# Optimization experiments

Hardware: AMD Instinct MI355X
Metric: run time of the kernel (lower is better)

Reference implementation:

```python
import jax, jax.numpy as jnp
import numpy as np

CHEB_K = 3
ORDER = 2


def setup_inputs() -> dict:
    key = jax.random.key(0)
    ks = jax.random.split(key, 7)
    B, C, N, T = 16, 64, 2048, 12
    E, O = 10, 64
    x = jax.random.normal(ks[0], (B, C, N, T), jnp.float32)
    node_embeddings = jax.random.normal(ks[1], (N, E), jnp.float32)
    # nonnegative row-normalized adjacency for the diffusion branch
    a = jax.random.uniform(ks[2], (1, N, N), jnp.float32)
    support = a / jnp.sum(a, axis=-1, keepdims=True)
    weights_pool = 0.05 * jax.random.normal(ks[3], (E, CHEB_K, C, O), jnp.float32)
    bias_pool = 0.05 * jax.random.normal(ks[4], (E, O), jnp.float32)
    mlp_w = 0.05 * jax.random.normal(ks[5], ((ORDER * 1 + 1) * C, O), jnp.float32)
    mlp_b = 0.05 * jax.random.normal(ks[6], (O,), jnp.float32)
    return {
        "x": x,
        "node_embeddings": node_embeddings,
        "support": support,
        "weights_pool": weights_pool,
        "bias_pool": bias_pool,
        "mlp_w": mlp_w,
        "mlp_b": mlp_b,
    }


def reference(x, node_embeddings, support, weights_pool, bias_pool, mlp_w, mlp_b):
    # ---- adaptive Chebyshev branch ----
    N = node_embeddings.shape[0]
    A = jax.nn.softmax(jax.nn.relu(node_embeddings @ node_embeddings.T), axis=1)  # [N,N]
    supports = [jnp.eye(N, dtype=A.dtype), A]
    for _ in range(2, CHEB_K):
        supports.append(2.0 * (A @ supports[-1]) - supports[-2])
    S = jnp.stack(supports, axis=0)                         # [K,N,N]
    weights = jnp.einsum('nd,dkio->nkio', node_embeddings, weights_pool)  # [N,K,C,O]
    bias = node_embeddings @ bias_pool                      # [N,O]
    # x: [B,C,N,T]; diffuse then contract per-node weights
    x_g = jnp.einsum('knm,bimw->bwnki', S, x)               # [B,T,N,K,C]
    x_av = jnp.einsum('bwnki,nkio->bwno', x_g, weights) + bias  # [B,T,N,O]
    x_av = x_av.transpose(0, 3, 2, 1)                       # [B,O,N,T]

    # ---- diffusion conv branch ----
    out = [x]
    for si in range(support.shape[0]):
        a = support[si]                                     # [N,N]
        x1 = jnp.einsum('bcvl,vw->bcwl', x, a)
        out.append(x1)
        for _ in range(2, ORDER + 1):
            x1 = jnp.einsum('bcvl,vw->bcwl', x1, a)
            out.append(x1)
    xg = jnp.concatenate(out, axis=1)                       # [B,(order*S+1)*C,N,T]
    # 1x1 Conv2d == channel matmul; dropout is identity in eval mode
    x_gcn = jnp.einsum('bcnw,co->bonw', xg, mlp_w) + mlp_b[None, :, None, None]
    return x_av, x_gcn
```

## Files before the change

kernel.cpp:

```cpp
#include <hip/hip_runtime.h>
#include <stdint.h>

#define NN    2048
#define BB    16
#define CC    64
#define TT    12
#define OO    64
#define ED    10
#define JJ    12288
#define NJ    25165824
#define KC    192
#define NTK   32

typedef __attribute__((ext_vector_type(8))) short short8;
typedef __attribute__((ext_vector_type(4))) float f32x4;

__device__ __forceinline__ unsigned short f2bf(float x) {
    union { float f; unsigned int u; } v; v.f = x;
    unsigned int r = (v.u + 0x7FFFu + ((v.u >> 16) & 1u)) >> 16;
    return (unsigned short)r;
}
__device__ __forceinline__ float bf2f(unsigned short h) {
    union { unsigned int u; float f; } v; v.u = ((unsigned int)h) << 16;
    return v.f;
}
__device__ __forceinline__ void async_cp16(const void* g, void* l) {
    __builtin_amdgcn_global_load_lds(
        (const __attribute__((address_space(1))) void*)(uintptr_t)g,
        (__attribute__((address_space(3))) void*)(uintptr_t)l, 16, 0, 0);
}

__global__ __launch_bounds__(256) void k_softmax_A(const float* __restrict__ E,
                                                   unsigned short* __restrict__ Abf) {
    int n = blockIdx.x, tid = threadIdx.x;
    __shared__ float row[NN];
    __shared__ float red[256];
    float en[ED];
#pragma unroll
    for (int d = 0; d < ED; ++d) en[d] = E[n * ED + d];
    float mx = 0.0f;
    for (int m = tid; m < NN; m += 256) {
        float s = 0.f;
#pragma unroll
        for (int d = 0; d < ED; ++d) s += en[d] * E[m * ED + d];
        s = fmaxf(s, 0.0f);
        row[m] = s;
        mx = fmaxf(mx, s);
    }
    red[tid] = mx; __syncthreads();
    for (int s = 128; s; s >>= 1) { if (tid < s) red[tid] = fmaxf(red[tid], red[tid + s]); __syncthreads(); }
    mx = red[0]; __syncthreads();
    float sum = 0.f;
    for (int m = tid; m < NN; m += 256) { float e = __expf(row[m] - mx); row[m] = e; sum += e; }
    red[tid] = sum; __syncthreads();
    for (int s = 128; s; s >>= 1) { if (tid < s) red[tid] += red[tid + s]; __syncthreads(); }
    float inv = 1.0f / red[0];
    for (int m = tid; m < NN; m += 256) Abf[(size_t)n * NN + m] = f2bf(row[m] * inv);
}

__global__ void k_trans_bf(const float* __restrict__ src, unsigned short* __restrict__ dst) {
    __shared__ float t[32][33];
    int tx = threadIdx.x, ty = threadIdx.y;
    int x0 = blockIdx.x * 32, y0 = blockIdx.y * 32;
#pragma unroll
    for (int i = 0; i < 4; ++i)
        t[ty + i * 8][tx] = src[(size_t)(y0 + ty + i * 8) * NN + x0 + tx];
    __syncthreads();
#pragma unroll
    for (int i = 0; i < 4; ++i)
        dst[(size_t)(x0 + ty + i * 8) * NN + y0 + tx] = f2bf(t[tx][ty + i * 8]);
}

__global__ __launch_bounds__(256) void k_make_X2b(const float* __restrict__ x,
                                                  unsigned short* __restrict__ X2,
                                                  unsigned short* __restrict__ X2t) {
    extern __shared__ float lx[];
    int b = blockIdx.x, n0 = blockIdx.y * 32, tid = threadIdx.x;
#pragma unroll
    for (int v = 0; v < 24; ++v) {
        int f4 = v * 256 + tid;
        int c = f4 / 96, r4 = f4 - c * 96;
        const float4* src = (const float4*)(x + ((size_t)(b * CC + c) * NN + n0) * TT) + r4;
        float4 val = *src;
#pragma unroll
        for (int u = 0; u < 4; ++u) {
            int idx = r4 * 4 + u;
            int n = idx / 12, t = idx - n * 12;
            lx[c * 417 + n * 13 + t] = ((const float*)&val)[u];
        }
    }
    __syncthreads();
#pragma unroll
    for (int v = 0; v < 12; ++v) {
        int flat = v * 256 + tid;
        int n = flat / 96, u8 = flat - n * 96;
        int jl = u8 * 8;
        int t = jl >> 6, c0 = jl & 63;
        unsigned short w[8];
#pragma unroll
        for (int e = 0; e < 8; ++e) w[e] = f2bf(lx[(c0 + e) * 417 + n * 13 + t]);
        *(short8*)&X2[(size_t)(n0 + n) * JJ + b * 768 + jl] = *(short8*)w;
    }
#pragma unroll
    for (int v = 0; v < 12; ++v) {
        int flat = v * 256 + tid;
        int jl = flat >> 2, nq = (flat & 3) * 8;
        int t = jl >> 6, c = jl & 63;
        unsigned short w[8];
#pragma unroll
        for (int e = 0; e < 8; ++e) w[e] = f2bf(lx[c * 417 + (nq + e) * 13 + t]);
        *(short8*)&X2t[(size_t)(b * 768 + jl) * NN + n0 + nq] = *(short8*)w;
    }
}

__global__ __launch_bounds__(256) void k_trans16(const unsigned short* __restrict__ src,
                                                 unsigned short* __restrict__ dst) {
    __shared__ unsigned short t[64][72];
    int tid = threadIdx.x;
    int j0 = blockIdx.x * 64, n0 = blockIdx.y * 64;
    int r = tid >> 3, c8 = (tid & 7) * 8;
#pragma unroll
    for (int it = 0; it < 2; ++it) {
        int rr = r + it * 32;
        *(short8*)&t[rr][c8] = *(const short8*)&src[(size_t)(n0 + rr) * JJ + j0 + c8];
    }
    __syncthreads();
#pragma unroll
    for (int it = 0; it < 2; ++it) {
        int rr = r + it * 32;
        unsigned short v[8];
#pragma unroll
        for (int u = 0; u < 8; ++u) v[u] = t[c8 + u][rr];
        *(short8*)&dst[(size_t)(j0 + rr) * NN + n0 + c8] = *(short8*)v;
    }
}

template <int AOFF, int BOFF>
__device__ __forceinline__ void mfma_quad(f32x4 (&acc)[8][4],
                                          const short8 (&A)[4][2],
                                          const short8 (&B)[2][2]) {
    __builtin_amdgcn_s_setprio(1);
#pragma unroll
    for (int h = 0; h < 2; ++h)
#pragma unroll
        for (int tm = 0; tm < 4; ++tm)
#pragma unroll
            for (int tn = 0; tn < 2; ++tn)
                acc[AOFF + tm][BOFF + tn] = __builtin_amdgcn_mfma_f32_16x16x32_bf16(
                    A[tm][h], B[tn][h], acc[AOFF + tm][BOFF + tn], 0, 0, 0);
    __builtin_amdgcn_s_setprio(0);
}

__global__ __launch_bounds__(512, 2) void k_gemm8(const unsigned short* __restrict__ AmA,
                                                  const unsigned short* __restrict__ AmB,
                                                  const unsigned short* __restrict__ Bt,
                                                  unsigned short* __restrict__ OutA,
                                                  unsigned short* __restrict__ OutB) {
    extern __shared__ char ldsc[];
    int tid = threadIdx.x, lane = tid & 63, wv = tid >> 6;
    int q = lane >> 4, l15 = lane & 15;

    const unsigned short* Am = blockIdx.z ? AmB : AmA;
    unsigned short* Out      = blockIdx.z ? OutB : OutA;

    int j0g = blockIdx.x * 256, m0g = blockIdx.y * 256;

    int wmw = (wv >> 2) * 128;
    int wnw = (wv & 3) * 64;

    int srow = tid >> 3;
    int scol = ((tid & 7) * 16) ^ ((srow & 7) << 4);
    const char* srcA0 = (const char*)Am + (size_t)(m0g + srow) * 4096 + scol;
    const char* srcB0 = (const char*)Bt + (size_t)(j0g + srow) * 4096 + scol;
    char* dstA0 = ldsc + tid * 16;
    char* dstB0 = ldsc + 32768 + tid * 16;

#define STAGE_A(nb, kt, h)                                                                  \
    do {                                                                                    \
        async_cp16(srcA0 + (size_t)(kt) * 128 + (h) * 524288,                               \
                   dstA0 + (nb) * 65536 + (h) * 16384);                                     \
        async_cp16(srcA0 + (size_t)(kt) * 128 + (h) * 524288 + 262144,                      \
                   dstA0 + (nb) * 65536 + (h) * 16384 + 8192);                              \
    } while (0)
#define STAGE_B(nb, kt, h)                                                                  \
    do {                                                                                    \
        async_cp16(srcB0 + (size_t)(kt) * 128 + (h) * 524288,                               \
                   dstB0 + (nb) * 65536 + (h) * 16384);                                     \
        async_cp16(srcB0 + (size_t)(kt) * 128 + (h) * 524288 + 262144,                      \
                   dstB0 + (nb) * 65536 + (h) * 16384 + 8192);                              \
    } while (0)

    int rsw = (l15 & 7) << 4;
    int colh0 = (q * 16) ^ rsw;
    int colh1 = colh0 ^ 64;
    int arA = (wmw + l15) * 128;
    int arB = (wnw + l15) * 128;

    f32x4 acc[8][4];
#pragma unroll
    for (int a = 0; a < 8; ++a)
#pragma unroll
        for (int b = 0; b < 4; ++b) acc[a][b] = (f32x4){0.f, 0.f, 0.f, 0.f};

    STAGE_A(0, 0, 0);
    STAGE_A(0, 0, 1);
    STAGE_B(0, 0, 0);
    STAGE_B(0, 0, 1);
    STAGE_B(1, 1, 0);
    STAGE_B(1, 1, 1);
    asm volatile("s_waitcnt vmcnt(4)" ::: "memory");
    __builtin_amdgcn_s_barrier();
    asm volatile("" ::: "memory");

    int cur = 0;
    for (int t = 0; t < NTK; ++t, cur ^= 1) {
        const int nb = cur ^ 1;
        const char* pa = ldsc + (cur << 16);
        const char* pA0 = pa + arA;
        const char* pB0 = pa + 32768 + arB;

        if (t + 1 < NTK) {
            STAGE_A(nb, t + 1, 0);
            STAGE_A(nb, t + 1, 1);
        }

        short8 af[4][2], bf0[2][2], bf1[2][2];

#pragma unroll
        for (int tm = 0; tm < 4; ++tm) {
            af[tm][0] = *(const short8*)(pA0 + tm * 2048 + colh0);
            af[tm][1] = *(const short8*)(pA0 + tm * 2048 + colh1);
        }
#pragma unroll
        for (int tn = 0; tn < 2; ++tn) {
            bf0[tn][0] = *(const short8*)(pB0 + tn * 2048 + colh0);
            bf0[tn][1] = *(const short8*)(pB0 + tn * 2048 + colh1);
            bf1[tn][0] = *(const short8*)(pB0 + 4096 + tn * 2048 + colh0);
            bf1[tn][1] = *(const short8*)(pB0 + 4096 + tn * 2048 + colh1);
        }
        mfma_quad<0, 0>(acc, af, bf0);
        mfma_quad<0, 2>(acc, af, bf1);

        if (t + 2 < NTK) {
            asm volatile("s_waitcnt lgkmcnt(0)" ::: "memory");
            __builtin_amdgcn_s_barrier();
            asm volatile("" ::: "memory");
            STAGE_B(cur, t + 2, 0);
            STAGE_B(cur, t + 2, 1);
        }

#pragma unroll
        for (int tm = 0; tm < 4; ++tm) {
            af[tm][0] = *(const short8*)(pA0 + 8192 + tm * 2048 + colh0);
            af[tm][1] = *(const short8*)(pA0 + 8192 + tm * 2048 + colh1);
        }
        mfma_quad<4, 2>(acc, af, bf1);
        mfma_quad<4, 0>(acc, af, bf0);

        if (t + 2 < NTK) {
            asm volatile("s_waitcnt vmcnt(4) lgkmcnt(0)" ::: "memory");
            __builtin_amdgcn_s_barrier();
            asm volatile("" ::: "memory");
        } else if (t + 1 < NTK) {
            asm volatile("s_waitcnt vmcnt(0) lgkmcnt(0)" ::: "memory");
            __builtin_amdgcn_s_barrier();
            asm volatile("" ::: "memory");
        }
    }
#undef STAGE_A
#undef STAGE_B

#pragma unroll
    for (int a = 0; a < 8; ++a) {
        int mbase = m0g + wmw + (a >> 2) * 64 + (a & 3) * 16 + q * 4;
#pragma unroll
        for (int b = 0; b < 4; ++b) {
            int jj = j0g + wnw + (b >> 1) * 32 + (b & 1) * 16 + l15;
#pragma unroll
            for (int r = 0; r < 4; ++r) {
                size_t oidx = (size_t)(mbase + r) * JJ + jj;
                Out[oidx] = f2bf(acc[a][b][r]);
            }
        }
    }
}

__global__ __launch_bounds__(256) void k_node(const unsigned short* __restrict__ S0,
                                              const unsigned short* __restrict__ S1,
                                              const unsigned short* __restrict__ S2,
                                              const float* __restrict__ E,
                                              const float* __restrict__ Wp,
                                              const float* __restrict__ bias_pool,
                                              const float* __restrict__ mlp_w,
                                              const float* __restrict__ mlp_b,
                                              float* __restrict__ out,
                                              int branch) {
    int n = blockIdx.x, tid = threadIdx.x, lane = tid & 63, wv = tid >> 6;
    __shared__ __align__(16) unsigned short lW[64 * 200];
    __shared__ __align__(16) unsigned short lS[192 * 72];
    __shared__ float lBias[64];
    int q = lane >> 4, l15 = lane & 15;

    if (branch == 0) {
        float en[ED];
#pragma unroll
        for (int d = 0; d < ED; ++d) en[d] = E[n * ED + d];
        for (int idx = tid; idx < KC * OO; idx += 256) {
            int o = idx & 63, kap = idx >> 6;
            int k = kap >> 6, i = kap & 63;
            float s = 0.f;
#pragma unroll
            for (int d = 0; d < ED; ++d) {
                float w;
                if (k == 0)
                    w = Wp[((size_t)d * KC + i) * OO + o] - Wp[((size_t)d * KC + 128 + i) * OO + o];
                else if (k == 1)
                    w = Wp[((size_t)d * KC + 64 + i) * OO + o];
                else
                    w = 2.0f * Wp[((size_t)d * KC + 128 + i) * OO + o];
                s += en[d] * w;
            }
            lW[o * 200 + kap] = f2bf(s);
        }
        if (tid < 64) {
            float s = 0.f;
#pragma unroll
            for (int d = 0; d < ED; ++d) s += en[d] * bias_pool[d * OO + tid];
            lBias[tid] = s;
        }
    } else {
        for (int idx = tid; idx < KC * OO; idx += 256) {
            int o = idx & 63, kap = idx >> 6;
            lW[o * 200 + kap] = f2bf(mlp_w[kap * OO + o]);
        }
        if (tid < 64) lBias[tid] = mlp_b[tid];
    }

    f32x4 zero = {0.f, 0.f, 0.f, 0.f};
    f32x4 acc[3][4];
#pragma unroll
    for (int a = 0; a < 3; ++a)
#pragma unroll
        for (int b = 0; b < 4; ++b) acc[a][b] = zero;

    const unsigned short* Ss[3] = { S0 + (size_t)n * JJ, S1 + (size_t)n * JJ, S2 + (size_t)n * JJ };

    for (int s = 0; s < 3; ++s) {
        __syncthreads();
#pragma unroll
        for (int v = 0; v < 6; ++v) {
            int e8 = (v * 256 + tid) * 8;
            int m = e8 >> 6, i = e8 & 63;
            *(short8*)&lS[m * 72 + i] = *(const short8*)&Ss[s][e8];
        }
        __syncthreads();
#pragma unroll
        for (int h = 0; h < 2; ++h) {
            short8 af[3], bfr[4];
#pragma unroll
            for (int tm = 0; tm < 3; ++tm)
                af[tm] = *(const short8*)&lS[(wv * 48 + tm * 16 + l15) * 72 + h * 32 + q * 8];
#pragma unroll
            for (int tn = 0; tn < 4; ++tn)
                bfr[tn] = *(const short8*)&lW[(tn * 16 + l15) * 200 + s * 64 + h * 32 + q * 8];
#pragma unroll
            for (int tm = 0; tm < 3; ++tm)
#pragma unroll
                for (int tn = 0; tn < 4; ++tn)
                    acc[tm][tn] = __builtin_amdgcn_mfma_f32_16x16x32_bf16(af[tm], bfr[tn], acc[tm][tn], 0, 0, 0);
        }
    }
#pragma unroll
    for (int tm = 0; tm < 3; ++tm) {
#pragma unroll
        for (int tn = 0; tn < 4; ++tn) {
            int o = tn * 16 + l15;
#pragma unroll
            for (int r = 0; r < 4; ++r) {
                int m = wv * 48 + tm * 16 + q * 4 + r;
                int b = m / TT, t = m - b * TT;
                out[(((size_t)b * OO + o) * NN + n) * TT + t] = acc[tm][tn][r] + lBias[o];
            }
        }
    }
}

extern "C" void kernel_launch(void* const* d_in, const int* in_sizes, int n_in,
                              void* d_out, int out_size, void* d_ws, size_t ws_size,
                              hipStream_t stream) {
    const float* x         = (const float*)d_in[0];
    const float* node_emb  = (const float*)d_in[1];
    const float* support   = (const float*)d_in[2];
    const float* wpool     = (const float*)d_in[3];
    const float* bpool     = (const float*)d_in[4];
    const float* mlp_w     = (const float*)d_in[5];
    const float* mlp_b     = (const float*)d_in[6];
    float* out             = (float*)d_out;

    unsigned short* Abf = (unsigned short*)d_ws;
    unsigned short* Atb = Abf + (size_t)NN * NN;
    unsigned short* b1  = Atb + (size_t)NN * NN;
    unsigned short* b2  = b1 + (size_t)NJ;
    unsigned short* b3  = b2 + (size_t)NJ;
    unsigned short* b4  = b3 + (size_t)NJ;
    unsigned short* b5  = b4 + (size_t)NJ;

    static int attr_done = 0;
    if (!attr_done) {
        hipFuncSetAttribute(reinterpret_cast<const void*>(k_gemm8),
                            hipFuncAttributeMaxDynamicSharedMemorySize, 131072);
        hipFuncSetAttribute(reinterpret_cast<const void*>(k_make_X2b),
                            hipFuncAttributeMaxDynamicSharedMemorySize, 106752);
        attr_done = 1;
    }

    dim3 gg13(48, 8, 2);
    dim3 gg1(48, 8, 1);
    dim3 gt(192, 32);

    k_softmax_A<<<NN, 256, 0, stream>>>(node_emb, Abf);
    k_trans_bf<<<dim3(64, 64), dim3(32, 8), 0, stream>>>(support, Atb);
    k_make_X2b<<<dim3(16, 64), 256, 106752, stream>>>(x, b2, b1);

    k_gemm8<<<gg13, 512, 131072, stream>>>(Abf, Atb, b1, b4, b5);

    k_trans16<<<gt, 256, 0, stream>>>(b4, b3);
    k_gemm8<<<gg1, 512, 131072, stream>>>(Abf, Abf, b3, b1, b1);
    k_node<<<NN, 256, 0, stream>>>(b2, b4, b1, node_emb, wpool, bpool, nullptr, nullptr,
                                   out, 0);

    k_trans16<<<gt, 256, 0, stream>>>(b5, b3);
    k_gemm8<<<gg1, 512, 131072, stream>>>(Atb, Atb, b3, b4, b4);
    k_node<<<NN, 256, 0, stream>>>(b2, b5, b4, nullptr, nullptr, nullptr, mlp_w, mlp_b,
                                   out + (size_t)NJ, 1);
}
```

Measured before the change: 1.153 ms.

## Precompute per-node weights in separate kernel and pipeline node-kernel staging with async LDS copies

Moves the per-node Chebyshev weight folding out of k_node into a new k_wfold kernel that writes all node weights to workspace as bf16, so k_node only loads them. k_node now stages the three support slices with async global-to-LDS copies in a XOR-swizzled layout, overlapping loads with MFMA work through double-buffering and explicit waitcnt/barriers. The output stores are vectorized to float4. The branch order is also reordered to reuse buffers. The cost is an extra kernel and a large extra workspace write/read of folded weights.

After: 966.3 us. 16.2% less time.

```diff
diff --git a/kernel.cpp b/kernel.cpp
--- a/kernel.cpp
+++ b/kernel.cpp
@@ -20,10 +20,6 @@
     unsigned int r = (v.u + 0x7FFFu + ((v.u >> 16) & 1u)) >> 16;
     return (unsigned short)r;
 }
-__device__ __forceinline__ float bf2f(unsigned short h) {
-    union { unsigned int u; float f; } v; v.u = ((unsigned int)h) << 16;
-    return v.f;
-}
 __device__ __forceinline__ void async_cp16(const void* g, void* l) {
     __builtin_amdgcn_global_load_lds(
         (const __attribute__((address_space(1))) void*)(uintptr_t)g,
@@ -135,6 +131,38 @@
     }
 }
 
+__global__ __launch_bounds__(256) void k_wfold(const float* __restrict__ E,
+                                               const float* __restrict__ Wp,
+                                               unsigned short* __restrict__ Wall) {
+    __shared__ float lE[256 * ED];
+    int tid = threadIdx.x;
+    int col = blockIdx.x * 256 + tid;
+    int o = col / 192, kap = col - o * 192;
+    int n0 = blockIdx.y * 256;
+#pragma unroll
+    for (int v = 0; v < 10; ++v) lE[v * 256 + tid] = E[(size_t)n0 * ED + v * 256 + tid];
+    int k = kap >> 6, i = kap & 63;
+    float w[ED];
+#pragma unroll
+    for (int d = 0; d < ED; ++d) {
+        float v;
+        if (k == 0)
+            v = Wp[((size_t)d * KC + i) * OO + o] - Wp[((size_t)d * KC + 128 + i) * OO + o];
+        else if (k == 1)
+            v = Wp[((size_t)d * KC + 64 + i) * OO + o];
+        else
+            v = 2.0f * Wp[((size_t)d * KC + 128 + i) * OO + o];
+        w[d] = v;
+    }
+    __syncthreads();
+    for (int nn = 0; nn < 256; ++nn) {
+        float s = 0.f;
+#pragma unroll
+        for (int d = 0; d < ED; ++d) s += lE[nn * ED + d] * w[d];
+        Wall[(size_t)(n0 + nn) * 12288 + col] = f2bf(s);
+    }
+}
+
 template <int AOFF, int BOFF>
 __device__ __forceinline__ void mfma_quad(f32x4 (&acc)[8][4],
                                           const short8 (&A)[4][2],
@@ -151,6 +179,7 @@
     __builtin_amdgcn_s_setprio(0);
 }
 
+template <int TAG>
 __global__ __launch_bounds__(512, 2) void k_gemm8(const unsigned short* __restrict__ AmA,
                                                   const unsigned short* __restrict__ AmB,
                                                   const unsigned short* __restrict__ Bt,
@@ -285,47 +314,82 @@
     }
 }
 
+struct NodeFrags { short8 a[3][2], b[4][2]; };
+
+__device__ __forceinline__ void node_stage(const unsigned short* src, char* dst, int tid) {
+#pragma unroll
+    for (int v = 0; v < 6; ++v) {
+        int id = v * 256 + tid;
+        int m = id >> 3, c = id & 7;
+        async_cp16((const char*)src + m * 128 + ((c * 16) ^ ((m & 7) << 4)),
+                   dst + id * 16);
+    }
+}
+
+__device__ __forceinline__ void node_read(const char* pS, const unsigned short* lW,
+                                          int s, int wv, int q, int l15,
+                                          int colh0, int colh1, NodeFrags& f) {
+#pragma unroll
+    for (int tm = 0; tm < 3; ++tm) {
+        int rb = (wv * 48 + tm * 16 + l15) * 128;
+        f.a[tm][0] = *(const short8*)(pS + rb + colh0);
+        f.a[tm][1] = *(const short8*)(pS + rb + colh1);
+    }
+#pragma unroll
+    for (int tn = 0; tn < 4; ++tn) {
+        const unsigned short* wr = lW + (tn * 16 + l15) * 200 + s * 64 + q * 8;
+        f.b[tn][0] = *(const short8*)wr;
+        f.b[tn][1] = *(const short8*)(wr + 32);
+    }
+}
+
+__device__ __forceinline__ void node_mfma(f32x4 (&acc)[3][4], const NodeFrags& f) {
+#pragma unroll
+    for (int h = 0; h < 2; ++h)
+#pragma unroll
+        for (int tm = 0; tm < 3; ++tm)
+#pragma unroll
+            for (int tn = 0; tn < 4; ++tn)
+                acc[tm][tn] = __builtin_amdgcn_mfma_f32_16x16x32_bf16(
+                    f.a[tm][h], f.b[tn][h], acc[tm][tn], 0, 0, 0);
+}
+
+template <int BRANCH>
 __global__ __launch_bounds__(256) void k_node(const unsigned short* __restrict__ S0,
                                               const unsigned short* __restrict__ S1,
                                               const unsigned short* __restrict__ S2,
+                                              const unsigned short* __restrict__ Wall,
                                               const float* __restrict__ E,
-                                              const float* __restrict__ Wp,
                                               const float* __restrict__ bias_pool,
                                               const float* __restrict__ mlp_w,
                                               const float* __restrict__ mlp_b,
-                                              float* __restrict__ out,
-                                              int branch) {
+                                              float* __restrict__ out) {
+    extern __shared__ char lds[];
+    unsigned short* lW = (unsigned short*)lds;
+    char* lS0 = lds + 25600;
+    float* lBias = (float*)(lds + 74752);
+
     int n = blockIdx.x, tid = threadIdx.x, lane = tid & 63, wv = tid >> 6;
-    __shared__ __align__(16) unsigned short lW[64 * 200];
-    __shared__ __align__(16) unsigned short lS[192 * 72];
-    __shared__ float lBias[64];
     int q = lane >> 4, l15 = lane & 15;
-
-    if (branch == 0) {
-        float en[ED];
-#pragma unroll
-        for (int d = 0; d < ED; ++d) en[d] = E[n * ED + d];
-        for (int idx = tid; idx < KC * OO; idx += 256) {
-            int o = idx & 63, kap = idx >> 6;
-            int k = kap >> 6, i = kap & 63;
-            float s = 0.f;
-#pragma unroll
-            for (int d = 0; d < ED; ++d) {
-                float w;
-                if (k == 0)
-                    w = Wp[((size_t)d * KC + i) * OO + o] - Wp[((size_t)d * KC + 128 + i) * OO + o];
-                else if (k == 1)
-                    w = Wp[((size_t)d * KC + 64 + i) * OO + o];
-                else
-                    w = 2.0f * Wp[((size_t)d * KC + 128 + i) * OO + o];
-                s += en[d] * w;
-            }
-            lW[o * 200 + kap] = f2bf(s);
+    int colh0 = (q * 16) ^ ((l15 & 7) << 4);
+    int colh1 = colh0 ^ 64;
+
+    const unsigned short* Ss0 = S0 + (size_t)n * JJ;
+    const unsigned short* Ss1 = S1 + (size_t)n * JJ;
+    const unsigned short* Ss2 = S2 + (size_t)n * JJ;
+
+    if (BRANCH == 0) {
+#pragma unroll
+        for (int v = 0; v < 6; ++v) {
+            int idx = v * 256 + tid;
+            int o = idx / 24, k8 = idx - o * 24;
+            *(short8*)&lW[o * 200 + k8 * 8] =
+                *(const short8*)&Wall[(size_t)n * 12288 + (size_t)idx * 8];
         }
         if (tid < 64) {
             float s = 0.f;
 #pragma unroll
-            for (int d = 0; d < ED; ++d) s += en[d] * bias_pool[d * OO + tid];
+            for (int d = 0; d < ED; ++d) s += E[n * ED + d] * bias_pool[d * OO + tid];
             lBias[tid] = s;
         }
     } else {
@@ -336,51 +400,52 @@
         if (tid < 64) lBias[tid] = mlp_b[tid];
     }
 
-    f32x4 zero = {0.f, 0.f, 0.f, 0.f};
     f32x4 acc[3][4];
 #pragma unroll
     for (int a = 0; a < 3; ++a)
 #pragma unroll
-        for (int b = 0; b < 4; ++b) acc[a][b] = zero;
-
-    const unsigned short* Ss[3] = { S0 + (size_t)n * JJ, S1 + (size_t)n * JJ, S2 + (size_t)n * JJ };
-
-    for (int s = 0; s < 3; ++s) {
-        __syncthreads();
-#pragma unroll
-        for (int v = 0; v < 6; ++v) {
-            int e8 = (v * 256 + tid) * 8;
-            int m = e8 >> 6, i = e8 & 63;
-            *(short8*)&lS[m * 72 + i] = *(const short8*)&Ss[s][e8];
-        }
-        __syncthreads();
-#pragma unroll
-        for (int h = 0; h < 2; ++h) {
-            short8 af[3], bfr[4];
-#pragma unroll
-            for (int tm = 0; tm < 3; ++tm)
-                af[tm] = *(const short8*)&lS[(wv * 48 + tm * 16 + l15) * 72 + h * 32 + q * 8];
-#pragma unroll
-            for (int tn = 0; tn < 4; ++tn)
-                bfr[tn] = *(const short8*)&lW[(tn * 16 + l15) * 200 + s * 64 + h * 32 + q * 8];
-#pragma unroll
-            for (int tm = 0; tm < 3; ++tm)
-#pragma unroll
-                for (int tn = 0; tn < 4; ++tn)
-                    acc[tm][tn] = __builtin_amdgcn_mfma_f32_16x16x32_bf16(af[tm], bfr[tn], acc[tm][tn], 0, 0, 0);
-        }
-    }
+        for (int b = 0; b < 4; ++b) acc[a][b] = (f32x4){0.f, 0.f, 0.f, 0.f};
+
+    node_stage(Ss0, lS0, tid);
+    node_stage(Ss1, lS0 + 24576, tid);
+    asm volatile("s_waitcnt vmcnt(6) lgkmcnt(0)" ::: "memory");
+    __builtin_amdgcn_s_barrier();
+    asm volatile("" ::: "memory");
+
+    NodeFrags f;
+    node_read(lS0, lW, 0, wv, q, l15, colh0, colh1, f);
+    asm volatile("s_waitcnt lgkmcnt(0)" ::: "memory");
+    __builtin_amdgcn_s_barrier();
+    asm volatile("" ::: "memory");
+    node_stage(Ss2, lS0, tid);
+    node_mfma(acc, f);
+    asm volatile("s_waitcnt vmcnt(6)" ::: "memory");
+    __builtin_amdgcn_s_barrier();
+    asm volatile("" ::: "memory");
+
+    node_read(lS0 + 24576, lW, 1, wv, q, l15, colh0, colh1, f);
+    node_mfma(acc, f);
+    asm volatile("s_waitcnt vmcnt(0) lgkmcnt(0)" ::: "memory");
+    __builtin_amdgcn_s_barrier();
+    asm volatile("" ::: "memory");
+
+    node_read(lS0, lW, 2, wv, q, l15, colh0, colh1, f);
+    node_mfma(acc, f);
+
 #pragma unroll
     for (int tm = 0; tm < 3; ++tm) {
 #pragma unroll
         for (int tn = 0; tn < 4; ++tn) {
             int o = tn * 16 + l15;
-#pragma unroll
-            for (int r = 0; r < 4; ++r) {
-                int m = wv * 48 + tm * 16 + q * 4 + r;
-                int b = m / TT, t = m - b * TT;
-                out[(((size_t)b * OO + o) * NN + n) * TT + t] = acc[tm][tn][r] + lBias[o];
-            }
+            int m0 = wv * 48 + tm * 16 + q * 4;
+            int b = m0 / TT, t0 = m0 - b * TT;
+            float bias = lBias[o];
+            float4 vv;
+            vv.x = acc[tm][tn][0] + bias;
+            vv.y = acc[tm][tn][1] + bias;
+            vv.z = acc[tm][tn][2] + bias;
+            vv.w = acc[tm][tn][3] + bias;
+            *(float4*)&out[(((size_t)b * OO + o) * NN + n) * TT + t0] = vv;
         }
     }
 }
@@ -407,10 +472,18 @@
 
     static int attr_done = 0;
     if (!attr_done) {
-        hipFuncSetAttribute(reinterpret_cast<const void*>(k_gemm8),
+        hipFuncSetAttribute(reinterpret_cast<const void*>(k_gemm8<0>),
+                            hipFuncAttributeMaxDynamicSharedMemorySize, 131072);
+        hipFuncSetAttribute(reinterpret_cast<const void*>(k_gemm8<1>),
+                            hipFuncAttributeMaxDynamicSharedMemorySize, 131072);
+        hipFuncSetAttribute(reinterpret_cast<const void*>(k_gemm8<2>),
                             hipFuncAttributeMaxDynamicSharedMemorySize, 131072);
         hipFuncSetAttribute(reinterpret_cast<const void*>(k_make_X2b),
                             hipFuncAttributeMaxDynamicSharedMemorySize, 106752);
+        hipFuncSetAttribute(reinterpret_cast<const void*>(k_node<0>),
+                            hipFuncAttributeMaxDynamicSharedMemorySize, 75008);
+        hipFuncSetAttribute(reinterpret_cast<const void*>(k_node<1>),
+                            hipFuncAttributeMaxDynamicSharedMemorySize, 75008);
         attr_done = 1;
     }
 
@@ -422,15 +495,16 @@
     k_trans_bf<<<dim3(64, 64), dim3(32, 8), 0, stream>>>(support, Atb);
     k_make_X2b<<<dim3(16, 64), 256, 106752, stream>>>(x, b2, b1);
 
-    k_gemm8<<<gg13, 512, 131072, stream>>>(Abf, Atb, b1, b4, b5);
+    k_gemm8<0><<<gg13, 512, 131072, stream>>>(Abf, Atb, b1, b4, b5);
+
+    k_trans16<<<gt, 256, 0, stream>>>(b5, b3);
+    k_gemm8<1><<<gg1, 512, 131072, stream>>>(Atb, Atb, b3, b1, b1);
+    k_node<1><<<NN, 256, 75008, stream>>>(b2, b5, b1, b2, node_emb, bpool, mlp_w, mlp_b,
+                                          out + (size_t)NJ);
 
     k_trans16<<<gt, 256, 0, stream>>>(b4, b3);
-    k_gemm8<<<gg1, 512, 131072, stream>>>(Abf, Abf, b3, b1, b1);
-    k_node<<<NN, 256, 0, stream>>>(b2, b4, b1, node_emb, wpool, bpool, nullptr, nullptr,
-                                   out, 0);
-
-    k_trans16<<<gt, 256, 0, stream>>>(b5, b3);
-    k_gemm8<<<gg1, 512, 131072, stream>>>(Atb, Atb, b3, b4, b4);
-    k_node<<<NN, 256, 0, stream>>>(b2, b5, b4, nullptr, nullptr, nullptr, mlp_w, mlp_b,
-                                   out + (size_t)NJ, 1);
-}
+    k_gemm8<2><<<gg1, 512, 131072, stream>>>(Abf, Abf, b3, b5, b5);
+    k_wfold<<<dim3(48, 8), 256, 0, stream>>>(node_emb, wpool, b3);
+    k_node<0><<<NN, 256, 75008, stream>>>(b2, b4, b5, b3, node_emb, bpool, mlp_w, mlp_b,
+                                          out);
+}
```
